# Kernel optimization log

Measured on AMD Instinct MI355X. Metric: run time of the kernel, lower is better.

The kernel has to match this reference:

```python
import jax, jax.numpy as jnp
import numpy as np

D_MODEL = 1024
N_HEADS = 16
D_K = D_MODEL // N_HEADS  # 64
D_V = D_MODEL // N_HEADS  # 64
B, S = 2, 2048


def setup_inputs() -> dict:
    key = jax.random.key(0)
    ks = jax.random.split(key, 8)
    inp = {
        "Q": jax.random.normal(ks[0], (B, S, D_MODEL), dtype=jnp.float32),
        "K": jax.random.normal(ks[1], (B, S, D_MODEL), dtype=jnp.float32),
        "V": jax.random.normal(ks[2], (B, S, D_MODEL), dtype=jnp.float32),
        "prev": jax.random.normal(ks[3], (B, N_HEADS, S, S), dtype=jnp.float32) * 0.1,
        # torch nn.Linear weights are [out_features, in_features]
        "W_Q": jax.random.normal(ks[4], (N_HEADS * D_K, D_MODEL), dtype=jnp.float32) / np.sqrt(D_MODEL),
        "W_K": jax.random.normal(ks[5], (N_HEADS * D_K, D_MODEL), dtype=jnp.float32) / np.sqrt(D_MODEL),
        "W_V": jax.random.normal(ks[6], (N_HEADS * D_V, D_MODEL), dtype=jnp.float32) / np.sqrt(D_MODEL),
        "W_O": jax.random.normal(ks[7], (D_MODEL, N_HEADS * D_V), dtype=jnp.float32) / np.sqrt(N_HEADS * D_V),
    }
    return inp


def reference(Q, K, V, prev, W_Q, W_K, W_V, W_O):
    scale = D_K ** (-0.5)
    # projections: x @ W.T, then split heads -> (b, h, s, d)
    q = jnp.einsum('bsm,em->bse', Q, W_Q).reshape(B, S, N_HEADS, D_K).transpose(0, 2, 1, 3)
    k = jnp.einsum('bsm,em->bse', K, W_K).reshape(B, S, N_HEADS, D_K).transpose(0, 2, 1, 3)
    v = jnp.einsum('bsm,em->bse', V, W_V).reshape(B, S, N_HEADS, D_V).transpose(0, 2, 1, 3)
    scores = jnp.einsum('bhqd,bhkd->bhqk', q, k) * scale + prev
    attn = jax.nn.softmax(scores, axis=-1)  # attn_dropout = 0 (eval)
    context = jnp.einsum('bhqk,bhkd->bhqd', attn, v)
    context = context.transpose(0, 2, 1, 3).reshape(B, S, N_HEADS * D_V)
    output = jnp.einsum('bse,me->bsm', context, W_O)  # proj_dropout = 0 (eval)
    return (output, attn, scores)
```

## Files before the change

### kernel.cpp

```cpp
#include <hip/hip_runtime.h>

#define S_LEN 2048
#define NH 16
#define DH 64
#define DM 1024
#define NB 2
#define BS 4096

typedef __attribute__((ext_vector_type(4))) float f32x4;
typedef __attribute__((ext_vector_type(8))) short bfrag;

__device__ __forceinline__ unsigned short f2bf(float f) {
    unsigned u = __builtin_bit_cast(unsigned, f);
    u += 0x7FFFu + ((u >> 16) & 1u);
    return (unsigned short)(u >> 16);
}

__device__ __forceinline__ void bar_lgkm() {
    asm volatile("s_waitcnt lgkmcnt(0)" ::: "memory");
    __builtin_amdgcn_s_barrier();
}

__device__ __forceinline__ void gld16(const unsigned short* g, unsigned short* l) {
    __builtin_amdgcn_global_load_lds((const __attribute__((address_space(1))) void*)g,
                                     (__attribute__((address_space(3))) void*)l, 16, 0, 0);
}

__global__ __launch_bounds__(256) void cast_kernel(const float* __restrict__ in,
                                                   unsigned short* __restrict__ out, int n4) {
    int i = blockIdx.x * 256 + threadIdx.x;
    if (i < n4) {
        float4 v = reinterpret_cast<const float4*>(in)[i];
        ushort4 o;
        o.x = f2bf(v.x); o.y = f2bf(v.y); o.z = f2bf(v.z); o.w = f2bf(v.w);
        reinterpret_cast<ushort4*>(out)[i] = o;
    }
}

__global__ __launch_bounds__(256) void gemm_qkv(const unsigned short* __restrict__ Qc,
                                                const unsigned short* __restrict__ Kc,
                                                const unsigned short* __restrict__ Vc,
                                                const unsigned short* __restrict__ Wqc,
                                                const unsigned short* __restrict__ Wkc,
                                                const unsigned short* __restrict__ Wvc,
                                                unsigned short* __restrict__ qh,
                                                unsigned short* __restrict__ kh,
                                                unsigned short* __restrict__ vT) {
    const int z = blockIdx.z;
    const unsigned short* A = (z == 0) ? Qc : (z == 1) ? Kc : Vc;
    const unsigned short* B = (z == 0) ? Wqc : (z == 1) ? Wkc : Wvc;
    const int tid = threadIdx.x, lane = tid & 63;
    const int l15 = lane & 15, lhi = lane >> 4;
    const int w = tid >> 6, wr = w >> 1, wc = w & 1;
    const int m0 = blockIdx.y * 128, n0 = blockIdx.x * 128;
    const int K = DM;
    const int lr8 = lane >> 3;
    const int csw = (lane & 7) ^ lr8;

    __shared__ unsigned short sA[128 * 64];
    __shared__ unsigned short sB[128 * 64];

    f32x4 acc[4][4];
#pragma unroll
    for (int i = 0; i < 4; ++i)
#pragma unroll
        for (int j = 0; j < 4; ++j) acc[i][j] = (f32x4){0.f, 0.f, 0.f, 0.f};

    for (int t = 0; t < 16; ++t) {
        const int k0 = t * 64;
#pragma unroll
        for (int i = 0; i < 4; ++i) {
            int g = w * 4 + i;
            int row = g * 8 + lr8;
            gld16(A + (size_t)(m0 + row) * K + k0 + csw * 8, sA + g * 512);
            gld16(B + (size_t)(n0 + row) * K + k0 + csw * 8, sB + g * 512);
        }
        __syncthreads();
#pragma unroll
        for (int kk = 0; kk < 2; ++kk) {
            bfrag a[4], b[4];
#pragma unroll
            for (int f = 0; f < 4; ++f) {
                int ra = wr * 64 + f * 16 + l15;
                a[f] = *reinterpret_cast<const bfrag*>(
                    sA + ra * 64 + (((kk * 4 + lhi) ^ (ra & 7)) << 3));
                int rb = wc * 64 + f * 16 + l15;
                b[f] = *reinterpret_cast<const bfrag*>(
                    sB + rb * 64 + (((kk * 4 + lhi) ^ (rb & 7)) << 3));
            }
#pragma unroll
            for (int fm = 0; fm < 4; ++fm)
#pragma unroll
                for (int fn = 0; fn < 4; ++fn)
                    acc[fm][fn] =
                        __builtin_amdgcn_mfma_f32_16x16x32_bf16(a[fm], b[fn], acc[fm][fn], 0, 0, 0);
        }
        __syncthreads();
    }

    if (z == 2) {
#pragma unroll
        for (int fm = 0; fm < 4; ++fm)
#pragma unroll
            for (int fn = 0; fn < 4; ++fn) {
                int sbase = m0 + wr * 64 + fm * 16 + (lhi << 2);
                int gcol = n0 + wc * 64 + fn * 16 + l15;
                int b = sbase >> 11, s = sbase & 2047, h = gcol >> 6, d = gcol & 63;
                ushort4 o;
                o.x = f2bf(acc[fm][fn][0]); o.y = f2bf(acc[fm][fn][1]);
                o.z = f2bf(acc[fm][fn][2]); o.w = f2bf(acc[fm][fn][3]);
                *reinterpret_cast<ushort4*>(vT + ((size_t)(b * NH + h) * DH + d) * S_LEN + s) = o;
            }
    } else {
        unsigned short* Out = (z == 0) ? qh : kh;
#pragma unroll
        for (int fm = 0; fm < 4; ++fm)
#pragma unroll
            for (int fn = 0; fn < 4; ++fn)
#pragma unroll
                for (int r = 0; r < 4; ++r) {
                    int grow = m0 + wr * 64 + fm * 16 + (lhi << 2) + r;
                    int gcol = n0 + wc * 64 + fn * 16 + l15;
                    int b = grow >> 11, s = grow & 2047, h = gcol >> 6, d = gcol & 63;
                    Out[((size_t)(b * NH + h) * S_LEN + s) * DH + d] = f2bf(acc[fm][fn][r]);
                }
    }
}

__global__ __launch_bounds__(256) void gemm_out(const unsigned short* __restrict__ A,
                                                const unsigned short* __restrict__ B,
                                                float* __restrict__ Out) {
    const int tid = threadIdx.x, lane = tid & 63;
    const int l15 = lane & 15, lhi = lane >> 4;
    const int w = tid >> 6, wr = w >> 1, wc = w & 1;
    const int m0 = blockIdx.y * 128, n0 = blockIdx.x * 128;
    const int K = DM, N = DM;
    const int lr8 = lane >> 3;
    const int csw = (lane & 7) ^ lr8;

    __shared__ unsigned short sA[128 * 64];
    __shared__ unsigned short sB[128 * 64];

    f32x4 acc[4][4];
#pragma unroll
    for (int i = 0; i < 4; ++i)
#pragma unroll
        for (int j = 0; j < 4; ++j) acc[i][j] = (f32x4){0.f, 0.f, 0.f, 0.f};

    for (int t = 0; t < 16; ++t) {
        const int k0 = t * 64;
#pragma unroll
        for (int i = 0; i < 4; ++i) {
            int g = w * 4 + i;
            int row = g * 8 + lr8;
            gld16(A + (size_t)(m0 + row) * K + k0 + csw * 8, sA + g * 512);
            gld16(B + (size_t)(n0 + row) * K + k0 + csw * 8, sB + g * 512);
        }
        __syncthreads();
#pragma unroll
        for (int kk = 0; kk < 2; ++kk) {
            bfrag a[4], b[4];
#pragma unroll
            for (int f = 0; f < 4; ++f) {
                int ra = wr * 64 + f * 16 + l15;
                a[f] = *reinterpret_cast<const bfrag*>(
                    sA + ra * 64 + (((kk * 4 + lhi) ^ (ra & 7)) << 3));
                int rb = wc * 64 + f * 16 + l15;
                b[f] = *reinterpret_cast<const bfrag*>(
                    sB + rb * 64 + (((kk * 4 + lhi) ^ (rb & 7)) << 3));
            }
#pragma unroll
            for (int fm = 0; fm < 4; ++fm)
#pragma unroll
                for (int fn = 0; fn < 4; ++fn)
                    acc[fm][fn] =
                        __builtin_amdgcn_mfma_f32_16x16x32_bf16(a[fm], b[fn], acc[fm][fn], 0, 0, 0);
        }
        __syncthreads();
    }

#pragma unroll
    for (int fm = 0; fm < 4; ++fm)
#pragma unroll
        for (int fn = 0; fn < 4; ++fn)
#pragma unroll
            for (int r = 0; r < 4; ++r) {
                int grow = m0 + wr * 64 + fm * 16 + (lhi << 2) + r;
                int gcol = n0 + wc * 64 + fn * 16 + l15;
                Out[(size_t)grow * N + gcol] = acc[fm][fn][r];
            }
}

__global__ __launch_bounds__(256, 4) void attn_fused(const unsigned short* __restrict__ qh,
                                                     const unsigned short* __restrict__ kh,
                                                     const unsigned short* __restrict__ vT,
                                                     const float* __restrict__ prev,
                                                     float* __restrict__ scores,
                                                     float* __restrict__ attn,
                                                     unsigned short* __restrict__ ctx) {
    const int z = blockIdx.z;
    const int m0 = blockIdx.x * 64;
    const int tid = threadIdx.x;
    const int lane = tid & 63;
    const int w = tid >> 6;
    const int l15 = lane & 15, lhi = lane >> 4;

    __shared__ unsigned short smem[16384];
    unsigned short* sQ = smem;
    unsigned short* sK = smem + 4096;
    unsigned short* sV = smem;
    unsigned short* sP = smem + 8192;

    const unsigned short* Qz = qh + (size_t)z * S_LEN * DH;
    const unsigned short* Kz = kh + (size_t)z * S_LEN * DH;
    const unsigned short* Vz = vT + (size_t)z * DH * S_LEN;
    const size_t zbase = (size_t)z * S_LEN * S_LEN;
    const float scale = 0.125f;
    const int rowb = w * 16 + lhi * 4;

#pragma unroll
    for (int i = 0; i < 2; ++i) {
        int c = i * 256 + tid, row = c >> 3, col8 = c & 7;
        *reinterpret_cast<int4*>(sQ + row * 64 + ((col8 * 8) ^ ((row & 7) * 8))) =
            *reinterpret_cast<const int4*>(Qz + (size_t)(m0 + row) * DH + col8 * 8);
    }

    float m_r[4], l_r[4];
#pragma unroll
    for (int r = 0; r < 4; ++r) { m_r[r] = -1e30f; l_r[r] = 0.f; }

    int4 kreg[4];
#pragma unroll
    for (int i = 0; i < 4; ++i) {
        int c = i * 256 + tid, row = c >> 3, col8 = c & 7;
        kreg[i] = *reinterpret_cast<const int4*>(Kz + (size_t)row * DH + col8 * 8);
    }
    float pv[32];
#pragma unroll
    for (int fn = 0; fn < 8; ++fn)
#pragma unroll
        for (int r = 0; r < 4; ++r)
            pv[fn * 4 + r] = __builtin_nontemporal_load(
                prev + zbase + (size_t)(m0 + rowb + r) * S_LEN + fn * 16 + l15);

    for (int kt = 0; kt < S_LEN / 128; ++kt) {
        const int n0 = kt * 128;
        bar_lgkm();
#pragma unroll
        for (int i = 0; i < 4; ++i) {
            int c = i * 256 + tid, row = c >> 3, col8 = c & 7;
            *reinterpret_cast<int4*>(sK + row * 64 + ((col8 * 8) ^ ((row & 7) * 8))) = kreg[i];
        }
        if (kt < 15) {
            const int n1 = n0 + 128;
#pragma unroll
            for (int i = 0; i < 4; ++i) {
                int c = i * 256 + tid, row = c >> 3, col8 = c & 7;
                kreg[i] = *reinterpret_cast<const int4*>(Kz + (size_t)(n1 + row) * DH + col8 * 8);
            }
        }
        bar_lgkm();

        f32x4 acc[8];
#pragma unroll
        for (int fn = 0; fn < 8; ++fn) acc[fn] = (f32x4){0.f, 0.f, 0.f, 0.f};
#pragma unroll
        for (int kk = 0; kk < 2; ++kk) {
            int ra = w * 16 + l15;
            bfrag a = *reinterpret_cast<const bfrag*>(sQ + ra * 64 +
                                                      ((kk * 32 + lhi * 8) ^ ((ra & 7) * 8)));
            bfrag b[8];
#pragma unroll
            for (int f = 0; f < 8; ++f) {
                int rb = f * 16 + l15;
                b[f] = *reinterpret_cast<const bfrag*>(sK + rb * 64 +
                                                       ((kk * 32 + lhi * 8) ^ ((rb & 7) * 8)));
            }
#pragma unroll
            for (int fn = 0; fn < 8; ++fn)
                acc[fn] = __builtin_amdgcn_mfma_f32_16x16x32_bf16(a, b[fn], acc[fn], 0, 0, 0);
        }

#pragma unroll
        for (int fn = 0; fn < 8; ++fn)
#pragma unroll
            for (int r = 0; r < 4; ++r) acc[fn][r] = acc[fn][r] * scale + pv[fn * 4 + r];
        if (kt < 15) {
            const int n1 = n0 + 128;
#pragma unroll
            for (int fn = 0; fn < 8; ++fn)
#pragma unroll
                for (int r = 0; r < 4; ++r)
                    pv[fn * 4 + r] = __builtin_nontemporal_load(
                        prev + zbase + (size_t)(m0 + rowb + r) * S_LEN + n1 + fn * 16 + l15);
        }
#pragma unroll
        for (int fn = 0; fn < 8; ++fn)
#pragma unroll
            for (int r = 0; r < 4; ++r)
                scores[zbase + (size_t)(m0 + rowb + r) * S_LEN + n0 + fn * 16 + l15] = acc[fn][r];
#pragma unroll
        for (int r = 0; r < 4; ++r) {
            float pm = acc[0][r];
#pragma unroll
            for (int fn = 1; fn < 8; ++fn) pm = fmaxf(pm, acc[fn][r]);
            pm = fmaxf(pm, __shfl_xor(pm, 1));
            pm = fmaxf(pm, __shfl_xor(pm, 2));
            pm = fmaxf(pm, __shfl_xor(pm, 4));
            pm = fmaxf(pm, __shfl_xor(pm, 8));
            float mnew = fmaxf(m_r[r], pm);
            float psum = 0.f;
#pragma unroll
            for (int fn = 0; fn < 8; ++fn) psum += __expf(acc[fn][r] - mnew);
            psum += __shfl_xor(psum, 1);
            psum += __shfl_xor(psum, 2);
            psum += __shfl_xor(psum, 4);
            psum += __shfl_xor(psum, 8);
            l_r[r] = l_r[r] * __expf(m_r[r] - mnew) + psum;
            m_r[r] = mnew;
        }
    }

    float inv_l[4];
#pragma unroll
    for (int r = 0; r < 4; ++r) inv_l[r] = 1.0f / l_r[r];

    f32x4 acco[4];
#pragma unroll
    for (int fn = 0; fn < 4; ++fn) acco[fn] = (f32x4){0.f, 0.f, 0.f, 0.f};

    int4 vreg[4];
#pragma unroll
    for (int i = 0; i < 4; ++i) {
        int c = i * 256 + tid, row = c >> 4, col8 = c & 15;
        vreg[i] = *reinterpret_cast<const int4*>(Vz + (size_t)row * S_LEN + col8 * 8);
    }
    float sv[32];
#pragma unroll
    for (int fn = 0; fn < 8; ++fn)
#pragma unroll
        for (int r = 0; r < 4; ++r)
            sv[fn * 4 + r] = scores[zbase + (size_t)(m0 + rowb + r) * S_LEN + fn * 16 + l15];

    for (int kt = 0; kt < S_LEN / 128; ++kt) {
        const int n0 = kt * 128;
        bar_lgkm();
#pragma unroll
        for (int i = 0; i < 4; ++i) {
            int c = i * 256 + tid, row = c >> 4, col8 = c & 15;
            *reinterpret_cast<int4*>(sV + row * 128 + ((col8 ^ (row & 7)) << 3)) = vreg[i];
        }
        if (kt < 15) {
            const int n1 = n0 + 128;
#pragma unroll
            for (int i = 0; i < 4; ++i) {
                int c = i * 256 + tid, row = c >> 4, col8 = c & 15;
                vreg[i] = *reinterpret_cast<const int4*>(Vz + (size_t)row * S_LEN + n1 + col8 * 8);
            }
        }
#pragma unroll
        for (int fn = 0; fn < 8; ++fn)
#pragma unroll
            for (int r = 0; r < 4; ++r) {
                float p = __expf(sv[fn * 4 + r] - m_r[r]) * inv_l[r];
                __builtin_nontemporal_store(
                    p, attn + zbase + (size_t)(m0 + rowb + r) * S_LEN + n0 + fn * 16 + l15);
                int prow = rowb + r, pcol = fn * 16 + l15;
                sP[prow * 128 + (((pcol >> 3) ^ (prow & 7)) << 3) + (pcol & 7)] = f2bf(p);
            }
        if (kt < 15) {
            const int n1 = n0 + 128;
#pragma unroll
            for (int fn = 0; fn < 8; ++fn)
#pragma unroll
                for (int r = 0; r < 4; ++r)
                    sv[fn * 4 + r] =
                        scores[zbase + (size_t)(m0 + rowb + r) * S_LEN + n1 + fn * 16 + l15];
        }
        bar_lgkm();
#pragma unroll
        for (int kk = 0; kk < 4; ++kk) {
            int ra = w * 16 + l15;
            bfrag a = *reinterpret_cast<const bfrag*>(sP + ra * 128 +
                                                      (((kk * 4 + lhi) ^ (ra & 7)) << 3));
            bfrag b[4];
#pragma unroll
            for (int f = 0; f < 4; ++f) {
                int rb = f * 16 + l15;
                b[f] = *reinterpret_cast<const bfrag*>(sV + rb * 128 +
                                                       (((kk * 4 + lhi) ^ (rb & 7)) << 3));
            }
#pragma unroll
            for (int fn = 0; fn < 4; ++fn)
                acco[fn] = __builtin_amdgcn_mfma_f32_16x16x32_bf16(a, b[fn], acco[fn], 0, 0, 0);
        }
    }

    const int b = z >> 4, h = z & 15;
#pragma unroll
    for (int fn = 0; fn < 4; ++fn)
#pragma unroll
        for (int r = 0; r < 4; ++r) {
            int s = m0 + rowb + r;
            int d = fn * 16 + l15;
            ctx[((size_t)(b * S_LEN + s)) * DM + h * DH + d] = f2bf(acco[fn][r]);
        }
}

extern "C" void kernel_launch(void* const* d_in, const int* in_sizes, int n_in, void* d_out,
                              int out_size, void* d_ws, size_t ws_size, hipStream_t stream) {
    const float* Q = (const float*)d_in[0];
    const float* K = (const float*)d_in[1];
    const float* V = (const float*)d_in[2];
    const float* prev = (const float*)d_in[3];
    const float* Wq = (const float*)d_in[4];
    const float* Wk = (const float*)d_in[5];
    const float* Wv = (const float*)d_in[6];
    const float* Wo = (const float*)d_in[7];

    float* out = (float*)d_out;
    float* attn = out + (size_t)BS * DM;
    float* scores = attn + (size_t)NB * NH * S_LEN * S_LEN;

    unsigned short* ws = (unsigned short*)d_ws;
    unsigned short* Qc = ws;
    unsigned short* Kc = Qc + (size_t)BS * DM;
    unsigned short* Vc = Kc + (size_t)BS * DM;
    unsigned short* Wqc = Vc + (size_t)BS * DM;
    unsigned short* Wkc = Wqc + (size_t)DM * DM;
    unsigned short* Wvc = Wkc + (size_t)DM * DM;
    unsigned short* Woc = Wvc + (size_t)DM * DM;
    unsigned short* qh = Woc + (size_t)DM * DM;
    unsigned short* kh = qh + (size_t)BS * DM;
    unsigned short* vT = kh + (size_t)BS * DM;
    unsigned short* ctx = vT + (size_t)BS * DM;

    cast_kernel<<<BS * DM / 4 / 256, 256, 0, stream>>>(Q, Qc, BS * DM / 4);
    cast_kernel<<<BS * DM / 4 / 256, 256, 0, stream>>>(K, Kc, BS * DM / 4);
    cast_kernel<<<BS * DM / 4 / 256, 256, 0, stream>>>(V, Vc, BS * DM / 4);
    cast_kernel<<<DM * DM / 4 / 256, 256, 0, stream>>>(Wq, Wqc, DM * DM / 4);
    cast_kernel<<<DM * DM / 4 / 256, 256, 0, stream>>>(Wk, Wkc, DM * DM / 4);
    cast_kernel<<<DM * DM / 4 / 256, 256, 0, stream>>>(Wv, Wvc, DM * DM / 4);
    cast_kernel<<<DM * DM / 4 / 256, 256, 0, stream>>>(Wo, Woc, DM * DM / 4);

    dim3 gq(DM / 128, BS / 128, 3);
    gemm_qkv<<<gq, 256, 0, stream>>>(Qc, Kc, Vc, Wqc, Wkc, Wvc, qh, kh, vT);

    dim3 ga(S_LEN / 64, 1, NB * NH);
    attn_fused<<<ga, 256, 0, stream>>>(qh, kh, vT, prev, scores, attn, ctx);

    dim3 gp(DM / 128, BS / 128, 1);
    gemm_out<<<gp, 256, 0, stream>>>(ctx, Woc, out);
}
```

Before: 727.9 us.

## Transpose MFMA operands so each lane owns one query row with vector accesses

Swaps the A/B operands of the QK^T and PV MFMAs so the accumulator holds 4 consecutive key columns of a single query row per lane. Loads of prev, stores of scores and attn, and the ctx writes become 16-byte or 8-byte vector accesses instead of scalar strided ones. Softmax state collapses to one row per lane, and the row reductions need only two cross-lane shuffles instead of four. The PV pass now walks the key tiles in reverse order so it starts on the most recently written scores, which are more likely to still be in cache.

```diff
diff --git a/kernel.cpp b/kernel.cpp
--- a/kernel.cpp
+++ b/kernel.cpp
@@ -216,7 +216,12 @@
     const unsigned short* Vz = vT + (size_t)z * DH * S_LEN;
     const size_t zbase = (size_t)z * S_LEN * S_LEN;
     const float scale = 0.125f;
-    const int rowb = w * 16 + lhi * 4;
+
+    const int qrow = w * 16 + l15;
+    const float* prevRow = prev + zbase + (size_t)(m0 + qrow) * S_LEN;
+    float* scoresRow = scores + zbase + (size_t)(m0 + qrow) * S_LEN;
+    float* attnRow = attn + zbase + (size_t)(m0 + qrow) * S_LEN;
+    const int c4 = lhi * 4;
 
 #pragma unroll
     for (int i = 0; i < 2; ++i) {
@@ -225,9 +230,7 @@
             *reinterpret_cast<const int4*>(Qz + (size_t)(m0 + row) * DH + col8 * 8);
     }
 
-    float m_r[4], l_r[4];
-#pragma unroll
-    for (int r = 0; r < 4; ++r) { m_r[r] = -1e30f; l_r[r] = 0.f; }
+    float m_r = -1e30f, l_r = 0.f;
 
     int4 kreg[4];
 #pragma unroll
@@ -235,13 +238,11 @@
         int c = i * 256 + tid, row = c >> 3, col8 = c & 7;
         kreg[i] = *reinterpret_cast<const int4*>(Kz + (size_t)row * DH + col8 * 8);
     }
-    float pv[32];
+    f32x4 pv4[8];
 #pragma unroll
     for (int fn = 0; fn < 8; ++fn)
-#pragma unroll
-        for (int r = 0; r < 4; ++r)
-            pv[fn * 4 + r] = __builtin_nontemporal_load(
-                prev + zbase + (size_t)(m0 + rowb + r) * S_LEN + fn * 16 + l15);
+        pv4[fn] = __builtin_nontemporal_load(
+            reinterpret_cast<const f32x4*>(prevRow + fn * 16 + c4));
 
     for (int kt = 0; kt < S_LEN / 128; ++kt) {
         const int n0 = kt * 128;
@@ -266,64 +267,55 @@
         for (int fn = 0; fn < 8; ++fn) acc[fn] = (f32x4){0.f, 0.f, 0.f, 0.f};
 #pragma unroll
         for (int kk = 0; kk < 2; ++kk) {
-            int ra = w * 16 + l15;
-            bfrag a = *reinterpret_cast<const bfrag*>(sQ + ra * 64 +
-                                                      ((kk * 32 + lhi * 8) ^ ((ra & 7) * 8)));
-            bfrag b[8];
+            bfrag qf = *reinterpret_cast<const bfrag*>(
+                sQ + qrow * 64 + (((kk * 4 + lhi) ^ (qrow & 7)) << 3));
+            bfrag kf[8];
 #pragma unroll
             for (int f = 0; f < 8; ++f) {
                 int rb = f * 16 + l15;
-                b[f] = *reinterpret_cast<const bfrag*>(sK + rb * 64 +
-                                                       ((kk * 32 + lhi * 8) ^ ((rb & 7) * 8)));
+                kf[f] = *reinterpret_cast<const bfrag*>(
+                    sK + rb * 64 + (((kk * 4 + lhi) ^ (rb & 7)) << 3));
             }
 #pragma unroll
             for (int fn = 0; fn < 8; ++fn)
-                acc[fn] = __builtin_amdgcn_mfma_f32_16x16x32_bf16(a, b[fn], acc[fn], 0, 0, 0);
+                acc[fn] = __builtin_amdgcn_mfma_f32_16x16x32_bf16(kf[fn], qf, acc[fn], 0, 0, 0);
         }
 
 #pragma unroll
         for (int fn = 0; fn < 8; ++fn)
 #pragma unroll
-            for (int r = 0; r < 4; ++r) acc[fn][r] = acc[fn][r] * scale + pv[fn * 4 + r];
+            for (int r = 0; r < 4; ++r) acc[fn][r] = acc[fn][r] * scale + pv4[fn][r];
         if (kt < 15) {
             const int n1 = n0 + 128;
 #pragma unroll
             for (int fn = 0; fn < 8; ++fn)
-#pragma unroll
-                for (int r = 0; r < 4; ++r)
-                    pv[fn * 4 + r] = __builtin_nontemporal_load(
-                        prev + zbase + (size_t)(m0 + rowb + r) * S_LEN + n1 + fn * 16 + l15);
+                pv4[fn] = __builtin_nontemporal_load(
+                    reinterpret_cast<const f32x4*>(prevRow + n1 + fn * 16 + c4));
         }
 #pragma unroll
         for (int fn = 0; fn < 8; ++fn)
-#pragma unroll
-            for (int r = 0; r < 4; ++r)
-                scores[zbase + (size_t)(m0 + rowb + r) * S_LEN + n0 + fn * 16 + l15] = acc[fn][r];
-#pragma unroll
-        for (int r = 0; r < 4; ++r) {
-            float pm = acc[0][r];
-#pragma unroll
-            for (int fn = 1; fn < 8; ++fn) pm = fmaxf(pm, acc[fn][r]);
-            pm = fmaxf(pm, __shfl_xor(pm, 1));
-            pm = fmaxf(pm, __shfl_xor(pm, 2));
-            pm = fmaxf(pm, __shfl_xor(pm, 4));
-            pm = fmaxf(pm, __shfl_xor(pm, 8));
-            float mnew = fmaxf(m_r[r], pm);
-            float psum = 0.f;
-#pragma unroll
-            for (int fn = 0; fn < 8; ++fn) psum += __expf(acc[fn][r] - mnew);
-            psum += __shfl_xor(psum, 1);
-            psum += __shfl_xor(psum, 2);
-            psum += __shfl_xor(psum, 4);
-            psum += __shfl_xor(psum, 8);
-            l_r[r] = l_r[r] * __expf(m_r[r] - mnew) + psum;
-            m_r[r] = mnew;
-        }
-    }
-
-    float inv_l[4];
-#pragma unroll
-    for (int r = 0; r < 4; ++r) inv_l[r] = 1.0f / l_r[r];
+            *reinterpret_cast<f32x4*>(scoresRow + n0 + fn * 16 + c4) = acc[fn];
+
+        float pm = acc[0][0];
+#pragma unroll
+        for (int fn = 0; fn < 8; ++fn)
+#pragma unroll
+            for (int r = 0; r < 4; ++r) pm = fmaxf(pm, acc[fn][r]);
+        pm = fmaxf(pm, __shfl_xor(pm, 16));
+        pm = fmaxf(pm, __shfl_xor(pm, 32));
+        float mnew = fmaxf(m_r, pm);
+        float psum = 0.f;
+#pragma unroll
+        for (int fn = 0; fn < 8; ++fn)
+#pragma unroll
+            for (int r = 0; r < 4; ++r) psum += __expf(acc[fn][r] - mnew);
+        psum += __shfl_xor(psum, 16);
+        psum += __shfl_xor(psum, 32);
+        l_r = l_r * __expf(m_r - mnew) + psum;
+        m_r = mnew;
+    }
+
+    const float inv_l = 1.0f / l_r;
 
     f32x4 acco[4];
 #pragma unroll
@@ -333,16 +325,14 @@
 #pragma unroll
     for (int i = 0; i < 4; ++i) {
         int c = i * 256 + tid, row = c >> 4, col8 = c & 15;
-        vreg[i] = *reinterpret_cast<const int4*>(Vz + (size_t)row * S_LEN + col8 * 8);
-    }
-    float sv[32];
+        vreg[i] = *reinterpret_cast<const int4*>(Vz + (size_t)row * S_LEN + 15 * 128 + col8 * 8);
+    }
+    f32x4 sv4[8];
 #pragma unroll
     for (int fn = 0; fn < 8; ++fn)
-#pragma unroll
-        for (int r = 0; r < 4; ++r)
-            sv[fn * 4 + r] = scores[zbase + (size_t)(m0 + rowb + r) * S_LEN + fn * 16 + l15];
-
-    for (int kt = 0; kt < S_LEN / 128; ++kt) {
+        sv4[fn] = *reinterpret_cast<const f32x4*>(scoresRow + 15 * 128 + fn * 16 + c4);
+
+    for (int kt = 15; kt >= 0; --kt) {
         const int n0 = kt * 128;
         bar_lgkm();
 #pragma unroll
@@ -350,8 +340,8 @@
             int c = i * 256 + tid, row = c >> 4, col8 = c & 15;
             *reinterpret_cast<int4*>(sV + row * 128 + ((col8 ^ (row & 7)) << 3)) = vreg[i];
         }
-        if (kt < 15) {
-            const int n1 = n0 + 128;
+        if (kt > 0) {
+            const int n1 = n0 - 128;
 #pragma unroll
             for (int i = 0; i < 4; ++i) {
                 int c = i * 256 + tid, row = c >> 4, col8 = c & 15;
@@ -359,52 +349,51 @@
             }
         }
 #pragma unroll
-        for (int fn = 0; fn < 8; ++fn)
-#pragma unroll
-            for (int r = 0; r < 4; ++r) {
-                float p = __expf(sv[fn * 4 + r] - m_r[r]) * inv_l[r];
-                __builtin_nontemporal_store(
-                    p, attn + zbase + (size_t)(m0 + rowb + r) * S_LEN + n0 + fn * 16 + l15);
-                int prow = rowb + r, pcol = fn * 16 + l15;
-                sP[prow * 128 + (((pcol >> 3) ^ (prow & 7)) << 3) + (pcol & 7)] = f2bf(p);
-            }
-        if (kt < 15) {
-            const int n1 = n0 + 128;
+        for (int fn = 0; fn < 8; ++fn) {
+            f32x4 p4;
+#pragma unroll
+            for (int r = 0; r < 4; ++r) p4[r] = __expf(sv4[fn][r] - m_r) * inv_l;
+            __builtin_nontemporal_store(p4,
+                                        reinterpret_cast<f32x4*>(attnRow + n0 + fn * 16 + c4));
+            ushort4 pb;
+            pb.x = f2bf(p4[0]); pb.y = f2bf(p4[1]); pb.z = f2bf(p4[2]); pb.w = f2bf(p4[3]);
+            int cch = (fn * 2 + (lhi >> 1)) ^ (qrow & 7);
+            *reinterpret_cast<ushort4*>(sP + qrow * 128 + cch * 8 + (lhi & 1) * 4) = pb;
+        }
+        if (kt > 0) {
+            const int n1 = n0 - 128;
 #pragma unroll
             for (int fn = 0; fn < 8; ++fn)
-#pragma unroll
-                for (int r = 0; r < 4; ++r)
-                    sv[fn * 4 + r] =
-                        scores[zbase + (size_t)(m0 + rowb + r) * S_LEN + n1 + fn * 16 + l15];
+                sv4[fn] = *reinterpret_cast<const f32x4*>(scoresRow + n1 + fn * 16 + c4);
         }
         bar_lgkm();
 #pragma unroll
         for (int kk = 0; kk < 4; ++kk) {
-            int ra = w * 16 + l15;
-            bfrag a = *reinterpret_cast<const bfrag*>(sP + ra * 128 +
-                                                      (((kk * 4 + lhi) ^ (ra & 7)) << 3));
-            bfrag b[4];
+            bfrag pf = *reinterpret_cast<const bfrag*>(
+                sP + qrow * 128 + (((kk * 4 + lhi) ^ (qrow & 7)) << 3));
+            bfrag vf[4];
 #pragma unroll
             for (int f = 0; f < 4; ++f) {
-                int rb = f * 16 + l15;
-                b[f] = *reinterpret_cast<const bfrag*>(sV + rb * 128 +
-                                                       (((kk * 4 + lhi) ^ (rb & 7)) << 3));
+                int rv = f * 16 + l15;
+                vf[f] = *reinterpret_cast<const bfrag*>(
+                    sV + rv * 128 + (((kk * 4 + lhi) ^ (rv & 7)) << 3));
             }
 #pragma unroll
             for (int fn = 0; fn < 4; ++fn)
-                acco[fn] = __builtin_amdgcn_mfma_f32_16x16x32_bf16(a, b[fn], acco[fn], 0, 0, 0);
+                acco[fn] = __builtin_amdgcn_mfma_f32_16x16x32_bf16(vf[fn], pf, acco[fn], 0, 0, 0);
         }
     }
 
     const int b = z >> 4, h = z & 15;
-#pragma unroll
-    for (int fn = 0; fn < 4; ++fn)
-#pragma unroll
-        for (int r = 0; r < 4; ++r) {
-            int s = m0 + rowb + r;
-            int d = fn * 16 + l15;
-            ctx[((size_t)(b * S_LEN + s)) * DM + h * DH + d] = f2bf(acco[fn][r]);
-        }
+    const int s = m0 + qrow;
+#pragma unroll
+    for (int fn = 0; fn < 4; ++fn) {
+        int d0 = fn * 16 + c4;
+        ushort4 o;
+        o.x = f2bf(acco[fn][0]); o.y = f2bf(acco[fn][1]);
+        o.z = f2bf(acco[fn][2]); o.w = f2bf(acco[fn][3]);
+        *reinterpret_cast<ushort4*>(ctx + ((size_t)(b * S_LEN + s)) * DM + h * DH + d0) = o;
+    }
 }
 
 extern "C" void kernel_launch(void* const* d_in, const int* in_sizes, int n_in, void* d_out,
```

New measurement: 671.1 us. 7.8% less time.
